# Kernel optimization log

Hardware: AMD Instinct MI355X
Metric: run time of the kernel (lower is better)

The kernel has to match this reference:

```python
import jax, jax.numpy as jnp
import numpy as np
from jax.scipy.stats import norm

H, W = 512, 512
HP, WP = 3, 3            # plane window
T_BINS, R_BINS = 180, 360  # accumulator dims (theta, rho)
THR_VAR = 100.0
ORIGIN = (0, 0)


def setup_inputs() -> dict:
    key = jax.random.key(0)
    k1, _ = jax.random.split(key)
    img = jax.random.uniform(k1, (H, W), dtype=jnp.float32)
    mask = jnp.ones((H, W), dtype=jnp.float32)
    return {"img": img, "mask": mask}


def _shift(img, dx, dy):
    # edge-clamped shifted view, matches xi = clip(hi+dx, 0, H-1)
    ri = jnp.clip(jnp.arange(H) + dx, 0, H - 1)
    ci = jnp.clip(jnp.arange(W) + dy, 0, W - 1)
    return img[ri][:, ci]


def reference(img, mask):
    img = img.astype(jnp.float32)
    dxs = range(-(HP // 2), HP // 2 + 1)
    dys = range(-(WP // 2), WP // 2 + 1)
    sum_x2 = float(sum(dx * dx for dx in dxs) * WP)  # = 6 for 3x3
    sum_y2 = float(sum(dy * dy for dy in dys) * HP)
    n_win = float(HP * WP)

    # ---- local plane fit (vectorized over all pixels, loop over 9 offsets) ----
    alpha = jnp.zeros((H, W), jnp.float32)
    beta = jnp.zeros((H, W), jnp.float32)
    gamma = jnp.zeros((H, W), jnp.float32)
    for dx in dxs:
        for dy in dys:
            s = _shift(img, dx, dy)
            alpha = alpha + dx * s
            beta = beta + dy * s
            gamma = gamma + s
    alpha = alpha / sum_x2 + 1e-6
    beta = beta / sum_y2 + 1e-6
    gamma = gamma / n_win

    # ---- residual variance (faithful to source: uses img[xi, wi]) ----
    eps2 = jnp.zeros((H, W), jnp.float32)
    for dx in dxs:
        row_s = _shift(img, dx, 0)  # img[clip(hi+dx), wi]
        for dy in dys:
            r = row_s - alpha * dy - beta * dx - gamma
            eps2 = eps2 + r * r
    noise_var = eps2 / (n_win - 2.0)
    var_alpha = noise_var / sum_x2
    var_beta = noise_var / sum_y2
    covar_ab = jnp.zeros_like(noise_var)  # sum_xy == 0 for symmetric window

    # ---- polar coordinates + uncertainty propagation ----
    theta = jnp.arctan(beta / alpha)  # in (-pi/2, pi/2)
    xg = (jnp.arange(H, dtype=jnp.float32) - ORIGIN[0])[:, None]
    yg = (jnp.arange(W, dtype=jnp.float32) - ORIGIN[1])[None, :]
    ct, st = jnp.cos(theta), jnp.sin(theta)
    rho = xg * ct + yg * st
    g2 = (alpha * alpha + beta * beta)
    var_theta = (beta * beta * var_alpha + alpha * alpha * var_beta
                 - 2.0 * alpha * beta * covar_ab) / (g2 * g2)
    drho_dt = -xg * st + yg * ct
    var_rho = drho_dt * drho_dt * var_theta

    # ---- Gaussian soft-voting into the accumulator ----
    theta_min, theta_max = -np.pi / 2, np.pi / 2
    rho_max = float(np.sqrt(H ** 2 + W ** 2))
    rho_min = -rho_max
    t_bin = (theta_max - theta_min) / (T_BINS - 1)
    r_bin = (rho_max - rho_min) / (R_BINS - 1)
    # bin i covers [center - bin/2, center + bin/2]
    t_edges = theta_min + (jnp.arange(T_BINS + 1, dtype=jnp.float32) - 0.5) * t_bin
    r_edges = rho_min + (jnp.arange(R_BINS + 1, dtype=jnp.float32) - 0.5) * r_bin

    valid = ((var_theta <= THR_VAR) & (var_rho <= THR_VAR)).astype(jnp.float32) * mask

    P = H * W
    thf = theta.reshape(P)
    rhf = rho.reshape(P)
    sig_t = jnp.sqrt(var_theta + 1e-12).reshape(P)
    sig_r = jnp.sqrt(var_rho + 1e-12).reshape(P)
    vf = valid.reshape(P)

    # per-pixel probability mass in each theta / rho bin (marginal Gaussian CDFs)
    cdf_t = norm.cdf((t_edges[None, :] - thf[:, None]) / sig_t[:, None])  # (P, T+1)
    wt = (cdf_t[:, 1:] - cdf_t[:, :-1]) * vf[:, None]                    # (P, T)
    cdf_r = norm.cdf((r_edges[None, :] - rhf[:, None]) / sig_r[:, None])  # (P, R+1)
    wr = cdf_r[:, 1:] - cdf_r[:, :-1]                                     # (P, R)

    acc = jnp.einsum('pt,pr->tr', wt, wr)  # (T_BINS, R_BINS) accumulated votes
    return acc
```

## Files before the change

### kernel.cpp

```cpp
#include <hip/hip_runtime.h>
#include <math.h>

#define H 512
#define W 512
#define TBINS 180
#define RBINS 360
#define NPIX (H*W)
#define NCELL (TBINS*RBINS)

#define THETA_MIN (-1.5707963267948966f)
#define T_BIN ((float)(3.141592653589793 / 179.0))
#define R_MIN (-724.0773439350246f)
#define R_BIN ((float)(2.0 * 724.0773439350246 / 359.0))
#define THR_VAR 100.0f
#define WSIG 6.0f

#define NT 6
#define KB 80
#define NBLK 1024
#define SCAP 256
#define MPAD 192

typedef short v8s __attribute__((ext_vector_type(8)));
typedef float v4f __attribute__((ext_vector_type(4)));

__device__ __forceinline__ float phi_cdf(float z) {
    return 0.5f * erfcf(-0.70710678118654752f * z);
}
__device__ __forceinline__ unsigned short f2bf(float f) {
    unsigned u = __float_as_uint(f);
    return (unsigned short)((u + 0x7FFF + ((u >> 16) & 1)) >> 16);
}
__device__ __forceinline__ float bf2f(unsigned short b) {
    return __uint_as_float(((unsigned)b) << 16);
}

__global__ void prep_kernel(const float* __restrict__ img,
                            const float* __restrict__ mask,
                            int* __restrict__ cblk,
                            float4* __restrict__ recs,
                            float* __restrict__ mvs,
                            float* __restrict__ out) {
    __shared__ int lcnt[NT];
    int tid = threadIdx.x;
    int b = blockIdx.x;
    int gid = b * blockDim.x + tid;
    if (gid < NCELL) out[gid] = 0.0f;
    if (tid < NT) lcnt[tid] = 0;
    __syncthreads();

    int p = gid;
    int hi = p >> 9, wi = p & (W - 1);
    float mv = mask[p];

    int xm = max(hi - 1, 0), xp = min(hi + 1, H - 1);
    int ym = max(wi - 1, 0), yp = min(wi + 1, W - 1);
    const float* r0 = img + xm * W;
    const float* r1 = img + hi * W;
    const float* r2 = img + xp * W;
    float s00 = r0[ym], s01 = r0[wi], s02 = r0[yp];
    float s10 = r1[ym], s11 = r1[wi], s12 = r1[yp];
    float s20 = r2[ym], s21 = r2[wi], s22 = r2[yp];

    float alpha_s = (s20 + s21 + s22) - (s00 + s01 + s02);
    float beta_s  = (s02 + s12 + s22) - (s00 + s10 + s20);
    float gsum    = s00 + s01 + s02 + s10 + s11 + s12 + s20 + s21 + s22;

    float alpha = alpha_s * (1.0f / 6.0f) + 1e-6f;
    float beta  = beta_s  * (1.0f / 6.0f) + 1e-6f;
    float gamma = gsum * (1.0f / 9.0f);

    float cvals[3] = { s01, s11, s21 };
    float eps2 = 0.0f;
    #pragma unroll
    for (int ix = 0; ix < 3; ++ix) {
        float dx = (float)(ix - 1);
        float c = cvals[ix];
        #pragma unroll
        for (int iy = 0; iy < 3; ++iy) {
            float dy = (float)(iy - 1);
            float r = c - alpha * dy - beta * dx - gamma;
            eps2 += r * r;
        }
    }
    float noise_var = eps2 * (1.0f / 7.0f);
    float va = noise_var * (1.0f / 6.0f);
    float g2 = alpha * alpha + beta * beta;
    float var_theta = (beta * beta * va + alpha * alpha * va) / (g2 * g2);

    float x = (float)hi, y = (float)wi;
    float inv_g = rsqrtf(g2);
    float cta = fabsf(alpha) * inv_g;
    float sta = (alpha < 0.0f ? -beta : beta) * inv_g;
    float drho_a = -x * sta + y * cta;
    float var_rho_a = drho_a * drho_a * var_theta;
    bool maybe = (var_theta <= THR_VAR) && (var_rho_a <= THR_VAR * 1.01f) && (mv != 0.0f);

    int myNt[2] = { -1, -1 };
    int myPos[2];
    float4 rc;
    if (maybe) {
        float theta = atanf(beta / alpha);
        float ct = cosf(theta), st = sinf(theta);
        float rho = x * ct + y * st;
        float drho = -x * st + y * ct;
        float var_rho = drho * drho * var_theta;
        if (var_rho <= THR_VAR) {
            float sig_t = sqrtf(var_theta + 1e-12f);
            float sig_r = sqrtf(var_rho + 1e-12f);
            float radr = WSIG * sig_r;
            int rlo = max((int)floorf((rho - radr - R_MIN) / R_BIN - 0.5f), 0);
            int rhi = min((int)ceilf((rho + radr - R_MIN) / R_BIN + 0.5f), RBINS - 1);
            if (rhi >= rlo) {
                rc.x = theta; rc.y = 1.0f / sig_t; rc.z = rho; rc.w = 1.0f / sig_r;
                int nt0 = rlo >> 6, nt1 = rhi >> 6;
                for (int nt = nt0; nt <= nt1; ++nt) {
                    int k = nt - nt0;
                    myNt[k] = nt;
                    myPos[k] = atomicAdd(&lcnt[nt], 1);
                }
            }
        }
    }
    __syncthreads();
    if (tid < NT) cblk[tid * NBLK + b] = lcnt[tid];
    #pragma unroll
    for (int k = 0; k < 2; ++k) {
        if (myNt[k] >= 0) {
            int idx = (myNt[k] * NBLK + b) * SCAP + myPos[k];
            recs[idx] = rc;
            mvs[idx]  = mv;
        }
    }
}

__global__ void __launch_bounds__(512)
gemm_kernel(const float4* __restrict__ recs,
            const float* __restrict__ mvs,
            const int* __restrict__ cblk,
            float* __restrict__ out) {
    __shared__ __align__(16) unsigned short Ah[MPAD * 32], Al[MPAD * 32];
    __shared__ __align__(16) unsigned short Bh[64 * 32],  Bl[64 * 32];
    __shared__ float4 prec[32];
    __shared__ float  pmv[32];
    __shared__ int    pref[NBLK];
    __shared__ int    wsum[8], woff[8];

    int nt = blockIdx.x % NT, kb = blockIdx.x / NT;
    int tid = threadIdx.x;
    int lane = tid & 63, wv = tid >> 6;
    int nsub = wv & 3, mhalf = wv >> 2;
    int c0 = nt * 64;
    int nbmax = min(63, RBINS - 1 - c0);

    const int* cb = cblk + nt * NBLK;
    int a0 = cb[2 * tid], a1 = cb[2 * tid + 1];
    int s = a0 + a1;
    #pragma unroll
    for (int d = 1; d < 64; d <<= 1) {
        int u = __shfl_up(s, d);
        if (lane >= d) s += u;
    }
    if (lane == 63) wsum[wv] = s;
    __syncthreads();
    if (tid == 0) {
        int r = 0;
        #pragma unroll
        for (int i = 0; i < 8; ++i) { woff[i] = r; r += wsum[i]; }
    }
    __syncthreads();
    int base = woff[wv] + s;
    pref[2 * tid]     = base - a1;
    pref[2 * tid + 1] = base;
    __syncthreads();

    int cn = pref[NBLK - 1];
    int nck = (cn + 31) >> 5;
    if (kb >= nck) return;

    v4f zero = {0.f, 0.f, 0.f, 0.f};
    v4f acc[6];
    #pragma unroll
    for (int i = 0; i < 6; ++i) acc[i] = zero;

    const float4* rb = recs + (size_t)nt * NBLK * SCAP;
    const float*  mb = mvs + (size_t)nt * NBLK * SCAP;

    int pix = tid & 31, g = tid >> 5;

    for (int ck = kb; ck < nck; ck += KB) {
        int k0 = ck << 5;
        int k1 = min(k0 + 32, cn);
        if (ck != kb) __syncthreads();
        if (tid < 32) {
            int r = k0 + tid;
            float4 rc; rc.x = 0.f; rc.y = 0.f; rc.z = 0.f; rc.w = 0.f;
            float m = 0.f;
            if (r < k1) {
                int pos = 0;
                #pragma unroll
                for (int st = 512; st >= 1; st >>= 1)
                    if (pos + st <= NBLK && pref[pos + st - 1] <= r) pos += st;
                int off = r - (pos ? pref[pos - 1] : 0);
                int idx = pos * SCAP + off;
                rc = rb[idx]; m = mb[idx];
            }
            prec[tid] = rc; pmv[tid] = m;
        }
        __syncthreads();

        float4 rc = prec[pix];
        float m = pmv[pix];
        float v[17];
        if (g < 12) {
            int e0 = g << 4;
            if (rc.y != 0.0f) {
                float sigt = 1.0f / rc.y;
                int wx = max((int)floorf((rc.x - WSIG * sigt - THETA_MIN) / T_BIN - 0.5f), 0);
                int wy = min((int)ceilf((rc.x + WSIG * sigt - THETA_MIN) / T_BIN + 0.5f), TBINS - 1);
                #pragma unroll
                for (int i = 0; i <= 16; ++i) {
                    int e = e0 + i;
                    float val;
                    if (e < wx) val = 0.0f;
                    else if (e > wy + 1) val = 1.0f;
                    else {
                        float edge = THETA_MIN + ((float)e - 0.5f) * T_BIN;
                        val = phi_cdf((edge - rc.x) * rc.y);
                    }
                    v[i] = val;
                }
            } else {
                #pragma unroll
                for (int i = 0; i <= 16; ++i) v[i] = 0.0f;
            }
            int sb = e0 * 32 + pix;
            #pragma unroll
            for (int i = 0; i < 16; ++i) {
                float wt = (v[i + 1] - v[i]) * m;
                unsigned short hb = f2bf(wt);
                Ah[sb + i * 32] = hb;
                Al[sb + i * 32] = f2bf(wt - bf2f(hb));
            }
        } else {
            int n0 = (g - 12) << 4;
            if (rc.y != 0.0f) {
                float sigr = 1.0f / rc.w;
                int wz = max((int)floorf((rc.z - WSIG * sigr - R_MIN) / R_BIN - 0.5f) - c0, 0);
                int ww = min((int)ceilf((rc.z + WSIG * sigr - R_MIN) / R_BIN + 0.5f) - c0, nbmax);
                #pragma unroll
                for (int i = 0; i <= 16; ++i) {
                    int n = n0 + i;
                    float val;
                    if (n < wz) val = 0.0f;
                    else if (n > ww + 1) val = 1.0f;
                    else {
                        float edge = R_MIN + ((float)(c0 + n) - 0.5f) * R_BIN;
                        val = phi_cdf((edge - rc.z) * rc.w);
                    }
                    v[i] = val;
                }
            } else {
                #pragma unroll
                for (int i = 0; i <= 16; ++i) v[i] = 0.0f;
            }
            int sb = n0 * 32 + pix;
            #pragma unroll
            for (int i = 0; i < 16; ++i) {
                float wr = v[i + 1] - v[i];
                unsigned short hb = f2bf(wr);
                Bh[sb + i * 32] = hb;
                Bl[sb + i * 32] = f2bf(wr - bf2f(hb));
            }
        }
        __syncthreads();

        int kq = (lane >> 4) * 8;
        int mr = lane & 15;
        v8s bh = *((__shared__ v8s*)&Bh[(nsub * 16 + mr) * 32 + kq]);
        v8s bl = *((__shared__ v8s*)&Bl[(nsub * 16 + mr) * 32 + kq]);
        #pragma unroll
        for (int mt = 0; mt < 6; ++mt) {
            int mbase = (mhalf * 6 + mt) * 16;
            v8s ah = *((__shared__ v8s*)&Ah[(mbase + mr) * 32 + kq]);
            v8s al = *((__shared__ v8s*)&Al[(mbase + mr) * 32 + kq]);
            acc[mt] = __builtin_amdgcn_mfma_f32_16x16x32_bf16(ah, bh, acc[mt], 0, 0, 0);
            acc[mt] = __builtin_amdgcn_mfma_f32_16x16x32_bf16(ah, bl, acc[mt], 0, 0, 0);
            acc[mt] = __builtin_amdgcn_mfma_f32_16x16x32_bf16(al, bh, acc[mt], 0, 0, 0);
        }
    }

    int gcol = c0 + nsub * 16 + (lane & 15);
    if (gcol < RBINS) {
        int rq = (lane >> 4) * 4;
        #pragma unroll
        for (int mt = 0; mt < 6; ++mt) {
            int rbase = (mhalf * 6 + mt) * 16 + rq;
            #pragma unroll
            for (int r = 0; r < 4; ++r) {
                int row = rbase + r;
                float v = acc[mt][r];
                if (row < TBINS && v != 0.0f)
                    atomicAdd(&out[row * RBINS + gcol], v);
            }
        }
    }
}

extern "C" void kernel_launch(void* const* d_in, const int* in_sizes, int n_in,
                              void* d_out, int out_size, void* d_ws, size_t ws_size,
                              hipStream_t stream) {
    const float* img  = (const float*)d_in[0];
    const float* mask = (const float*)d_in[1];
    float* out = (float*)d_out;

    char* ws = (char*)d_ws;
    int*    cblk = (int*)ws;
    float4* recs = (float4*)(ws + 32768);
    float*  mvs  = (float*)(ws + 32768 + (size_t)NT * NBLK * SCAP * 16);

    prep_kernel<<<NPIX / 256, 256, 0, stream>>>(img, mask, cblk, recs, mvs, out);
    gemm_kernel<<<NT * KB, 512, 0, stream>>>(recs, mvs, cblk, out);
}
```

Before: 83.79 us.

## Replace global atomic accumulation with per-block partial slabs and a reduce kernel

Each GEMM block now writes its full 192x64 accumulator tile to its own partial slab in workspace instead of issuing atomicAdds into the output. A new reduce kernel sums the active slabs per column tile, using the per-tile worker count stored by kb==0 blocks, and writes the output directly, so the output no longer needs zeroing in prep. This removes atomic contention on the output, but adds an extra kernel launch and extra global traffic for writing and rereading the partial slabs.

```diff
diff --git a/kernel.cpp b/kernel.cpp
--- a/kernel.cpp
+++ b/kernel.cpp
@@ -39,13 +39,11 @@
                             const float* __restrict__ mask,
                             int* __restrict__ cblk,
                             float4* __restrict__ recs,
-                            float* __restrict__ mvs,
-                            float* __restrict__ out) {
+                            float* __restrict__ mvs) {
     __shared__ int lcnt[NT];
     int tid = threadIdx.x;
     int b = blockIdx.x;
     int gid = b * blockDim.x + tid;
-    if (gid < NCELL) out[gid] = 0.0f;
     if (tid < NT) lcnt[tid] = 0;
     __syncthreads();
 
@@ -138,7 +136,8 @@
 gemm_kernel(const float4* __restrict__ recs,
             const float* __restrict__ mvs,
             const int* __restrict__ cblk,
-            float* __restrict__ out) {
+            int* __restrict__ nw,
+            float* __restrict__ part) {
     __shared__ __align__(16) unsigned short Ah[MPAD * 32], Al[MPAD * 32];
     __shared__ __align__(16) unsigned short Bh[64 * 32],  Bl[64 * 32];
     __shared__ float4 prec[32];
@@ -176,6 +175,7 @@
 
     int cn = pref[NBLK - 1];
     int nck = (cn + 31) >> 5;
+    if (kb == 0 && tid == 0) nw[nt] = min(nck, KB);
     if (kb >= nck) return;
 
     v4f zero = {0.f, 0.f, 0.f, 0.f};
@@ -290,21 +290,33 @@
         }
     }
 
-    int gcol = c0 + nsub * 16 + (lane & 15);
-    if (gcol < RBINS) {
-        int rq = (lane >> 4) * 4;
+    float* slab = part + (size_t)(nt * KB + kb) * (MPAD * 64);
+    int col = nsub * 16 + (lane & 15);
+    int rq = (lane >> 4) * 4;
+    #pragma unroll
+    for (int mt = 0; mt < 6; ++mt) {
+        int rbase = (mhalf * 6 + mt) * 16 + rq;
         #pragma unroll
-        for (int mt = 0; mt < 6; ++mt) {
-            int rbase = (mhalf * 6 + mt) * 16 + rq;
-            #pragma unroll
-            for (int r = 0; r < 4; ++r) {
-                int row = rbase + r;
-                float v = acc[mt][r];
-                if (row < TBINS && v != 0.0f)
-                    atomicAdd(&out[row * RBINS + gcol], v);
-            }
-        }
-    }
+        for (int r = 0; r < 4; ++r)
+            slab[(rbase + r) * 64 + col] = acc[mt][r];
+    }
+}
+
+__global__ void __launch_bounds__(64)
+reduce_kernel(const float4* __restrict__ part, const int* __restrict__ nw,
+              float4* __restrict__ out) {
+    int t = blockIdx.x / 45;
+    int q = (blockIdx.x % 45) * 64 + threadIdx.x;
+    int row = q >> 4, c4 = q & 15;
+    if (t == 5 && c4 >= 10) return;
+    int n = nw[t];
+    const float4* p = part + (size_t)t * KB * (MPAD * 16) + row * 16 + c4;
+    float4 s; s.x = 0.f; s.y = 0.f; s.z = 0.f; s.w = 0.f;
+    for (int j = 0; j < n; ++j) {
+        float4 v = p[(size_t)j * (MPAD * 16)];
+        s.x += v.x; s.y += v.y; s.z += v.z; s.w += v.w;
+    }
+    out[row * 90 + t * 16 + c4] = s;
 }
 
 extern "C" void kernel_launch(void* const* d_in, const int* in_sizes, int n_in,
@@ -315,10 +327,18 @@
     float* out = (float*)d_out;
 
     char* ws = (char*)d_ws;
+    size_t off_recs = 32768;
+    size_t off_mvs  = off_recs + (size_t)NT * NBLK * SCAP * 16;
+    size_t off_nw   = off_mvs + (size_t)NT * NBLK * SCAP * 4;
+    size_t off_part = off_nw + 1024;
+
     int*    cblk = (int*)ws;
-    float4* recs = (float4*)(ws + 32768);
-    float*  mvs  = (float*)(ws + 32768 + (size_t)NT * NBLK * SCAP * 16);
-
-    prep_kernel<<<NPIX / 256, 256, 0, stream>>>(img, mask, cblk, recs, mvs, out);
-    gemm_kernel<<<NT * KB, 512, 0, stream>>>(recs, mvs, cblk, out);
-}
+    float4* recs = (float4*)(ws + off_recs);
+    float*  mvs  = (float*)(ws + off_mvs);
+    int*    nw   = (int*)(ws + off_nw);
+    float*  part = (float*)(ws + off_part);
+
+    prep_kernel<<<NPIX / 256, 256, 0, stream>>>(img, mask, cblk, recs, mvs);
+    gemm_kernel<<<NT * KB, 512, 0, stream>>>(recs, mvs, cblk, nw, part);
+    reduce_kernel<<<270, 64, 0, stream>>>((const float4*)part, nw, (float4*)out);
+}
```

New measurement: 97.09 us. 1.16x slower.
